# Performance work log

Measured on AMD Instinct MI355X. Metric: run time of the kernel, lower is better.

The kernel has to match this reference:

```python
import jax, jax.numpy as jnp
import numpy as np
from jax import lax

WINDOW_SIZE = 11
SIGMA = 1.5
CHANNELS = 3


def _gaussian_window():
    # 2D gaussian kernel, normalized to sum 1, shape [C, 1, K, K] (OIHW depthwise)
    coords = jnp.arange(WINDOW_SIZE, dtype=jnp.float32) - WINDOW_SIZE // 2
    g2d = jnp.exp(-(coords[None, :] ** 2 + coords[:, None] ** 2) / (2.0 * SIGMA ** 2))
    g2d = g2d / g2d.sum()
    return jnp.broadcast_to(g2d[None, None], (CHANNELS, 1, WINDOW_SIZE, WINDOW_SIZE))


def _depthwise_blur(x, window):
    pad = WINDOW_SIZE // 2
    return lax.conv_general_dilated(
        x, window,
        window_strides=(1, 1),
        padding=[(pad, pad), (pad, pad)],
        dimension_numbers=("NCHW", "OIHW", "NCHW"),
        feature_group_count=CHANNELS,
    )


def setup_inputs() -> dict:
    key = jax.random.key(0)
    k1, k2 = jax.random.split(key)
    shape = (16, 3, 512, 512)
    img1 = jax.random.uniform(k1, shape, dtype=jnp.float32)
    img2 = jax.random.uniform(k2, shape, dtype=jnp.float32)
    return {"img1": img1, "img2": img2}


def reference(img1, img2):
    window = _gaussian_window()
    C1 = 0.01 ** 2
    C2 = 0.03 ** 2

    mu1 = _depthwise_blur(img1, window)
    mu2 = _depthwise_blur(img2, window)
    mu1_sq = mu1 * mu1
    mu2_sq = mu2 * mu2
    mu1_mu2 = mu1 * mu2

    sigma1_sq = _depthwise_blur(img1 * img1, window) - mu1_sq
    sigma2_sq = _depthwise_blur(img2 * img2, window) - mu2_sq
    sigma12 = _depthwise_blur(img1 * img2, window) - mu1_mu2

    ssim_map = ((2.0 * mu1_mu2 + C1) * (2.0 * sigma12 + C2)) / (
        (mu1_sq + mu2_sq + C1) * (sigma1_sq + sigma2_sq + C2)
    )
    # size_average=True -> scalar loss
    return 1.0 - ssim_map.mean()
```

## Files before the change

kernel.cpp:

```cpp
#include <hip/hip_runtime.h>

#define IMG 512
#define PAD 5
#define KW  11
#define SH  64
#define WCOLS 64
#define NWAVES 4
#define BW (WCOLS * NWAVES)
#define STG (WCOLS + 2 * PAD)
#define NPLANES 48
#define NCHUNK 7

__global__ __launch_bounds__(256, 4) void ssim_wave_kernel(
    const float* __restrict__ img1,
    const float* __restrict__ img2,
    double* __restrict__ accum)
{
    __shared__ float2 sbuf[NWAVES][STG + 1];

    float w[KW];
    {
        float wv[KW];
        float s = 0.f;
#pragma unroll
        for (int i = 0; i < KW; ++i) {
            float d = (float)(i - PAD);
            wv[i] = expf(-(d * d) / 4.5f);
            s += wv[i];
        }
#pragma unroll
        for (int i = 0; i < KW; ++i)
            w[i] = __uint_as_float(
                __builtin_amdgcn_readfirstlane(__float_as_uint(wv[i] / s)));
    }

    const int tid   = threadIdx.x;
    const int wv_id = tid >> 6;
    const int lane  = tid & 63;
    const int plane = blockIdx.z;
    const int wc0   = blockIdx.x * BW + wv_id * WCOLS;
    const int y0    = blockIdx.y * SH;

    const float* __restrict__ A = img1 + (size_t)plane * (IMG * IMG);
    const float* __restrict__ B = img2 + (size_t)plane * (IMG * IMG);
    float2* lbuf = &sbuf[wv_id][0];

    const int c0  = wc0 - PAD + lane;
    const int cc0 = min(max(c0, 0), IMG - 1);
    const float m0 = (c0 >= 0 && c0 < IMG) ? 1.f : 0.f;
    const int c1  = wc0 + (WCOLS - PAD) + lane;
    const int cc1 = min(c1, IMG - 1);
    const float m1 = (c1 < IMG) ? 1.f : 0.f;

    const int ystart = max(y0 - PAD, 0);
    const int yend   = min(y0 + SH + PAD, IMG);

    float acc0[KW], acc1[KW], acc2[KW], acc3[KW];
#pragma unroll
    for (int j = 0; j < KW; ++j) {
        acc0[j] = 0.f; acc1[j] = 0.f; acc2[j] = 0.f; acc3[j] = 0.f;
    }

    const float C1v = 1e-4f;
    const float C2v = 9e-4f;
    float local = 0.f;

    const float* rowA = A + (size_t)ystart * IMG;
    const float* rowB = B + (size_t)ystart * IMG;
    float pa0 = rowA[cc0], pb0 = rowB[cc0];
    float pa1 = rowA[cc1], pb1 = rowB[cc1];

    int y = ystart;

#define SSIM_EMIT(sd)                                                          \
    {                                                                          \
        const float mu1 = acc0[sd], mu2 = acc1[sd];                            \
        const float xs  = acc2[sd], x12 = acc3[sd];                            \
        const float mu1s = mu1 * mu1, mu2s = mu2 * mu2;                        \
        const float m12 = mu1 * mu2;                                           \
        const float num = (2.f * m12 + C1v) * (2.f * (x12 - m12) + C2v);       \
        const float den = (mu1s + mu2s + C1v) *                                \
                          ((xs - mu1s - mu2s) + C2v);                          \
        local += num * __builtin_amdgcn_rcpf(den);                             \
    }

#define SSIM_PHASE(p)                                                          \
    if (y < yend) {                                                            \
                  \
        lbuf[lane] = make_float2(pa0 * m0, pb0 * m0);                          \
        if (lane < 2 * PAD)                                                    \
            lbuf[WCOLS + lane] = make_float2(pa1 * m1, pb1 * m1);              \
               \
        if (y + 1 < yend) {                                                    \
            rowA += IMG; rowB += IMG;                                          \
            pa0 = rowA[cc0]; pb0 = rowB[cc0];                                  \
            pa1 = rowA[cc1]; pb1 = rowB[cc1];                                  \
        }                                                                      \
                            \
        float h0 = 0.f, h1 = 0.f, h2 = 0.f, h3 = 0.f;                          \
        _Pragma("unroll")                                                      \
        for (int k = 0; k < KW; ++k) {                                         \
            const float2 ab = lbuf[lane + k];                                  \
            const float a = ab.x, b = ab.y;                                    \
            float sq = a * a;                                                  \
            sq = fmaf(b, b, sq);                                               \
            h0 += w[k] * a;                                                    \
            h1 += w[k] * b;                                                    \
            h2 += w[k] * sq;                                                   \
            h3 += w[k] * (a * b);                                              \
        }                                                                      \
         \
        _Pragma("unroll")                                                      \
        for (int j = 0; j < KW; ++j) {                                         \
            const int sl = ((p) + 6 + j) % KW;                                 \
            const float wj = w[10 - j];                                        \
            acc0[sl] += wj * h0;                                               \
            acc1[sl] += wj * h1;                                               \
            acc2[sl] += wj * h2;                                               \
            acc3[sl] += wj * h3;                                               \
        }                                                                      \
                                        \
        {                                                                      \
            const int sd = ((p) + 6) % KW;                                     \
            const int r = y - PAD;                                             \
            if (r >= y0) SSIM_EMIT(sd);                                        \
            acc0[sd] = 0.f; acc1[sd] = 0.f; acc2[sd] = 0.f; acc3[sd] = 0.f;    \
        }                                                                      \
        ++y;                                                                   \
    }

#pragma unroll 1
    for (int chunk = 0; chunk < NCHUNK; ++chunk) {
        SSIM_PHASE(0) SSIM_PHASE(1) SSIM_PHASE(2) SSIM_PHASE(3)
        SSIM_PHASE(4) SSIM_PHASE(5) SSIM_PHASE(6) SSIM_PHASE(7)
        SSIM_PHASE(8) SSIM_PHASE(9) SSIM_PHASE(10)
    }
#undef SSIM_PHASE

    if (blockIdx.y == (IMG / SH - 1)) {
        SSIM_EMIT(9) SSIM_EMIT(10) SSIM_EMIT(0) SSIM_EMIT(1) SSIM_EMIT(2)
    }
#undef SSIM_EMIT

#pragma unroll
    for (int off = 32; off > 0; off >>= 1)
        local += __shfl_down(local, off);
    if (lane == 0)
        atomicAdd(accum, (double)local);
}

__global__ void ssim_finalize_kernel(const double* __restrict__ accum,
                                     float* __restrict__ out)
{
    const double N = (double)NPLANES * IMG * IMG;
    out[0] = (float)(1.0 - accum[0] / N);
}

extern "C" void kernel_launch(void* const* d_in, const int* in_sizes, int n_in,
                              void* d_out, int out_size, void* d_ws, size_t ws_size,
                              hipStream_t stream) {
    const float* img1 = (const float*)d_in[0];
    const float* img2 = (const float*)d_in[1];
    float* out = (float*)d_out;
    double* accum = (double*)d_ws;

    hipMemsetAsync(accum, 0, sizeof(double), stream);

    dim3 grid(IMG / BW, IMG / SH, NPLANES);
    ssim_wave_kernel<<<grid, BW, 0, stream>>>(img1, img2, accum);
    ssim_finalize_kernel<<<1, 1, 0, stream>>>(accum, out);
}
```

Before: 174.8 us.

## Pack SSIM blur accumulators into float2 vectors for packed FMA

Rewrites the separable blur so the four moment channels are held as two 2-wide float vectors (mu1/mu2 and a²+b²/2ab), with the aim of having the compiler emit packed FP32 FMAs (v_pk_fma_f32) and roughly halve VALU instruction count. The Gaussian weights become compile-time constants instead of being computed with expf at runtime, and the launch bound minimum occupancy drops from 4 to 2 blocks per CU to give more register room. The risk is that swizzle/shuffle overhead for building the packed operands, or lower occupancy, cancels the savings.

```diff
diff --git a/kernel.cpp b/kernel.cpp
--- a/kernel.cpp
+++ b/kernel.cpp
@@ -11,28 +11,22 @@
 #define NPLANES 48
 #define NCHUNK 7
 
-__global__ __launch_bounds__(256, 4) void ssim_wave_kernel(
+typedef float v2f __attribute__((ext_vector_type(2)));
+
+__global__ __launch_bounds__(256, 2) void ssim_pk_kernel(
     const float* __restrict__ img1,
     const float* __restrict__ img2,
     double* __restrict__ accum)
 {
-    __shared__ float2 sbuf[NWAVES][STG + 1];
+    __shared__ v2f sbuf[NWAVES][STG + 1];
 
-    float w[KW];
-    {
-        float wv[KW];
-        float s = 0.f;
-#pragma unroll
-        for (int i = 0; i < KW; ++i) {
-            float d = (float)(i - PAD);
-            wv[i] = expf(-(d * d) / 4.5f);
-            s += wv[i];
-        }
-#pragma unroll
-        for (int i = 0; i < KW; ++i)
-            w[i] = __uint_as_float(
-                __builtin_amdgcn_readfirstlane(__float_as_uint(wv[i] / s)));
-    }
+#define W0 0.00102837f
+#define W1 0.00759874f
+#define W2 0.03600077f
+#define W3 0.10936370f
+#define W4 0.21300551f
+#define W5 0.26601172f
+    static constexpr float WK[KW] = {W0, W1, W2, W3, W4, W5, W4, W3, W2, W1, W0};
 
     const int tid   = threadIdx.x;
     const int wv_id = tid >> 6;
@@ -43,7 +37,7 @@
 
     const float* __restrict__ A = img1 + (size_t)plane * (IMG * IMG);
     const float* __restrict__ B = img2 + (size_t)plane * (IMG * IMG);
-    float2* lbuf = &sbuf[wv_id][0];
+    v2f* lbuf = &sbuf[wv_id][0];
 
     const int c0  = wc0 - PAD + lane;
     const int cc0 = min(max(c0, 0), IMG - 1);
@@ -55,10 +49,11 @@
     const int ystart = max(y0 - PAD, 0);
     const int yend   = min(y0 + SH + PAD, IMG);
 
-    float acc0[KW], acc1[KW], acc2[KW], acc3[KW];
+    v2f rmu[KW], rx[KW];
 #pragma unroll
     for (int j = 0; j < KW; ++j) {
-        acc0[j] = 0.f; acc1[j] = 0.f; acc2[j] = 0.f; acc3[j] = 0.f;
+        rmu[j] = (v2f)0.f;
+        rx[j]  = (v2f)0.f;
     }
 
     const float C1v = 1e-4f;
@@ -74,57 +69,62 @@
 
 #define SSIM_EMIT(sd)                                                          \
     {                                                                          \
-        const float mu1 = acc0[sd], mu2 = acc1[sd];                            \
-        const float xs  = acc2[sd], x12 = acc3[sd];                            \
-        const float mu1s = mu1 * mu1, mu2s = mu2 * mu2;                        \
+        const float mu1 = rmu[sd].x, mu2 = rmu[sd].y;                          \
+        const float xs  = rx[sd].x,  x2ab = rx[sd].y;        \
         const float m12 = mu1 * mu2;                                           \
-        const float num = (2.f * m12 + C1v) * (2.f * (x12 - m12) + C2v);       \
-        const float den = (mu1s + mu2s + C1v) *                                \
-                          ((xs - mu1s - mu2s) + C2v);                          \
+        const float t2m = m12 + m12;                                           \
+        const float num = (t2m + C1v) * ((x2ab - t2m) + C2v);                  \
+        const float ssum = fmaf(mu1, mu1, mu2 * mu2);                          \
+        const float den = (ssum + C1v) * ((xs - ssum) + C2v);                  \
         local += num * __builtin_amdgcn_rcpf(den);                             \
     }
 
 #define SSIM_PHASE(p)                                                          \
     if (y < yend) {                                                            \
                   \
-        lbuf[lane] = make_float2(pa0 * m0, pb0 * m0);                          \
-        if (lane < 2 * PAD)                                                    \
-            lbuf[WCOLS + lane] = make_float2(pa1 * m1, pb1 * m1);              \
+        {                                                                      \
+            v2f st; st.x = pa0 * m0; st.y = pb0 * m0;                          \
+            lbuf[lane] = st;                                                   \
+            if (lane < 2 * PAD) {                                              \
+                v2f se; se.x = pa1 * m1; se.y = pb1 * m1;                      \
+                lbuf[WCOLS + lane] = se;                                       \
+            }                                                                  \
+        }                                                                      \
                \
         if (y + 1 < yend) {                                                    \
             rowA += IMG; rowB += IMG;                                          \
             pa0 = rowA[cc0]; pb0 = rowB[cc0];                                  \
             pa1 = rowA[cc1]; pb1 = rowB[cc1];                                  \
         }                                                                      \
-                            \
-        float h0 = 0.f, h1 = 0.f, h2 = 0.f, h3 = 0.f;                          \
+                                     \
+        v2f hmu = (v2f)0.f, hx = (v2f)0.f;                                     \
         _Pragma("unroll")                                                      \
         for (int k = 0; k < KW; ++k) {                                         \
-            const float2 ab = lbuf[lane + k];                                  \
-            const float a = ab.x, b = ab.y;                                    \
-            float sq = a * a;                                                  \
-            sq = fmaf(b, b, sq);                                               \
-            h0 += w[k] * a;                                                    \
-            h1 += w[k] * b;                                                    \
-            h2 += w[k] * sq;                                                   \
-            h3 += w[k] * (a * b);                                              \
+            const v2f ab = lbuf[lane + k];                       \
+            v2f aa;  aa.x = ab.x;  aa.y = ab.x;                  \
+            v2f byy; byy.x = ab.y; byy.y = ab.y;                 \
+            v2f byx; byx.x = ab.y; byx.y = ab.x;                 \
+            v2f u = aa * ab;                                     \
+            u = byy * byx + u;                               \
+            const v2f wk2 = {WK[k], WK[k]};                                    \
+            hmu = wk2 * ab + hmu;                                              \
+            hx  = wk2 * u  + hx;                                               \
         }                                                                      \
-         \
+           \
         _Pragma("unroll")                                                      \
         for (int j = 0; j < KW; ++j) {                                         \
             const int sl = ((p) + 6 + j) % KW;                                 \
-            const float wj = w[10 - j];                                        \
-            acc0[sl] += wj * h0;                                               \
-            acc1[sl] += wj * h1;                                               \
-            acc2[sl] += wj * h2;                                               \
-            acc3[sl] += wj * h3;                                               \
+            const v2f wj2 = {WK[j], WK[j]};     \
+            rmu[sl] = wj2 * hmu + rmu[sl];                                     \
+            rx[sl]  = wj2 * hx  + rx[sl];                                      \
         }                                                                      \
                                         \
         {                                                                      \
             const int sd = ((p) + 6) % KW;                                     \
             const int r = y - PAD;                                             \
             if (r >= y0) SSIM_EMIT(sd);                                        \
-            acc0[sd] = 0.f; acc1[sd] = 0.f; acc2[sd] = 0.f; acc3[sd] = 0.f;    \
+            rmu[sd] = (v2f)0.f;                                                \
+            rx[sd]  = (v2f)0.f;                                                \
         }                                                                      \
         ++y;                                                                   \
     }
@@ -167,6 +167,6 @@
     hipMemsetAsync(accum, 0, sizeof(double), stream);
 
     dim3 grid(IMG / BW, IMG / SH, NPLANES);
-    ssim_wave_kernel<<<grid, BW, 0, stream>>>(img1, img2, accum);
+    ssim_pk_kernel<<<grid, BW, 0, stream>>>(img1, img2, accum);
     ssim_finalize_kernel<<<1, 1, 0, stream>>>(accum, out);
 }
```

After: 175.8 us. No clear change (+0.6%).
